# Kernel optimization log

Hardware: AMD Instinct MI355X
Metric: run time of the kernel (lower is better)

## Reference

```python
import jax, jax.numpy as jnp
import numpy as np

N_NODES = 100000
N_EDGES = 1600000
D_IN = 256
H = 4       # n_heads
F = 64      # out_feats per head
NEG_SLOPE = 0.2


def setup_inputs() -> dict:
    key = jax.random.key(0)
    ks = jax.random.split(key, 8)
    feat = jax.random.normal(ks[0], (N_NODES, D_IN), dtype=jnp.float32)
    src = jax.random.randint(ks[1], (N_EDGES,), 0, N_NODES, dtype=jnp.int32)
    dst = jnp.sort(jax.random.randint(ks[2], (N_EDGES,), 0, N_NODES, dtype=jnp.int32))
    s = 1.0 / np.sqrt(D_IN)
    W_src = jax.random.normal(ks[3], (D_IN, H * F), dtype=jnp.float32) * s
    W_dst = jax.random.normal(ks[4], (D_IN, H * F), dtype=jnp.float32) * s
    b_dst = jnp.zeros((H * F,), dtype=jnp.float32)
    Wa_src = jax.random.normal(ks[5], (D_IN, H), dtype=jnp.float32) * s
    Wa_dst = jax.random.normal(ks[6], (D_IN, H), dtype=jnp.float32) * s
    return {"feat": feat, "W_src": W_src, "W_dst": W_dst, "b_dst": b_dst,
            "Wa_src": Wa_src, "Wa_dst": Wa_dst, "src": src, "dst": dst}


def reference(feat, W_src, W_dst, b_dst, Wa_src, Wa_dst, src, dst):
    N = feat.shape[0]
    # node projections
    h_src = (feat @ W_src).reshape(N, H, F)                  # [N,H,F]
    h_dst = (feat @ W_dst + b_dst).reshape(N, H, F)          # residual term
    a_src = feat @ Wa_src                                    # [N,H]
    a_dst = feat @ Wa_dst                                    # [N,H]
    # per-edge attention logits: u_add_v then leaky_relu
    e = a_src[src] + a_dst[dst]                              # [E,H]
    e = jnp.where(e > 0, e, NEG_SLOPE * e)
    # edge softmax grouped by destination node
    emax = jax.ops.segment_max(e, dst, num_segments=N)       # [N,H]
    emax = jnp.where(jnp.isfinite(emax), emax, 0.0)          # empty segments -> 0
    ex = jnp.exp(e - emax[dst])                              # [E,H]
    denom = jax.ops.segment_sum(ex, dst, num_segments=N)     # [N,H]
    a = ex / denom[dst]                                      # [E,H]
    # u_mul_e + sum aggregation
    msg = h_src[src] * a[:, :, None]                         # [E,H,F]
    out = jax.ops.segment_sum(msg, dst, num_segments=N)      # [N,H,F]
    return out + h_dst
```

## Files before the change

### kernel.cpp

```cpp
#include <hip/hip_runtime.h>

#define N_NODES 100000
#define N_EDGES 1600000
#define NEG_SLOPE 0.2f

typedef __bf16 bf16x8 __attribute__((ext_vector_type(8)));
typedef float f32x4 __attribute__((ext_vector_type(4)));
typedef _Float16 f16x4 __attribute__((ext_vector_type(4)));

__device__ inline unsigned short f2bf(float f) {
    union { float f; unsigned u; } x; x.f = f;
    unsigned r = x.u + 0x7fffu + ((x.u >> 16) & 1u);
    return (unsigned short)(r >> 16);
}

__global__ __launch_bounds__(256) void cvt_w_k(const float* __restrict__ Ws,
                                               const float* __restrict__ Wd,
                                               unsigned short* __restrict__ Wsw_src,
                                               unsigned short* __restrict__ Wsw_dst) {
    int idx = blockIdx.x * 256 + threadIdx.x;
    int sel = idx >> 16;
    int r = idx & 65535;
    int k = r >> 8, n = r & 255;
    int ct = n >> 4, nl = n & 15;
    int lane = ((k & 31) >> 3) * 16 + nl, j = k & 7;
    int ks = k >> 5;
    unsigned short v = f2bf((sel == 0 ? Ws : Wd)[k * 256 + n]);
    (sel == 0 ? Wsw_src : Wsw_dst)[(ct * 8 + ks) * 512 + lane * 8 + j] = v;
}

__global__ void cvt_wa_k(const float* __restrict__ Was,
                         const float* __restrict__ Wad,
                         unsigned short* __restrict__ Wa_sw) {
    int idx = blockIdx.x * 256 + threadIdx.x;
    int j = idx & 7, lane = (idx >> 3) & 63, ks = idx >> 9;
    int n = lane & 15, k = ks * 32 + (lane >> 4) * 8 + j;
    float v = n < 4 ? Was[k * 4 + n] : (n < 8 ? Wad[k * 4 + (n - 4)] : 0.f);
    Wa_sw[idx] = f2bf(v);
}

__global__ void rowptr_k(const int* __restrict__ dst, int* __restrict__ rp) {
    int n = blockIdx.x * 256 + threadIdx.x;
    if (n > N_NODES) return;
    int lo = 0, hi = N_EDGES;
    while (lo < hi) { int mid = (lo + hi) >> 1; if (dst[mid] < n) lo = mid + 1; else hi = mid; }
    rp[n] = lo;
}

__global__ __launch_bounds__(256) void aproj_k(const float* __restrict__ feat,
                                               const unsigned short* __restrict__ Wa_sw,
                                               _Float16* __restrict__ a_srcH,
                                               _Float16* __restrict__ a_dstH) {
    int wave = threadIdx.x >> 6, lane = threadIdx.x & 63;
    int quad = lane >> 4, l16 = lane & 15;
    int row_strip = (blockIdx.x * 4 + wave) * 16;
    int arow = row_strip + l16;
    if (arow >= N_NODES) arow = N_NODES - 1;
    const float* arow_p = feat + (size_t)arow * 256;
    const bf16x8* Wa8 = (const bf16x8*)Wa_sw;
    f32x4 acc = {0.f, 0.f, 0.f, 0.f};
    #pragma unroll
    for (int ks = 0; ks < 8; ++ks) {
        int k0 = ks * 32 + quad * 8;
        float4 f0 = *(const float4*)(arow_p + k0);
        float4 f1 = *(const float4*)(arow_p + k0 + 4);
        union { unsigned short u[8]; bf16x8 v; } cv;
        cv.u[0] = f2bf(f0.x); cv.u[1] = f2bf(f0.y);
        cv.u[2] = f2bf(f0.z); cv.u[3] = f2bf(f0.w);
        cv.u[4] = f2bf(f1.x); cv.u[5] = f2bf(f1.y);
        cv.u[6] = f2bf(f1.z); cv.u[7] = f2bf(f1.w);
        acc = __builtin_amdgcn_mfma_f32_16x16x32_bf16(cv.v, Wa8[ks * 64 + lane], acc, 0, 0, 0);
    }
    #pragma unroll
    for (int r = 0; r < 4; ++r) {
        int n = row_strip + quad * 4 + r;
        if (n < N_NODES) {
            if (l16 < 4)      a_srcH[(size_t)n * 4 + l16] = (_Float16)acc[r];
            else if (l16 < 8) a_dstH[(size_t)n * 4 + (l16 - 4)] = (_Float16)acc[r];
        }
    }
}

__global__ __launch_bounds__(512) void proj_k(const float* __restrict__ feat,
                                              const unsigned short* __restrict__ Wsw_src,
                                              const unsigned short* __restrict__ Wsw_dst,
                                              const float* __restrict__ b_dst,
                                              _Float16* __restrict__ h_src,
                                              float* __restrict__ out) {
    __shared__ unsigned short F[4 * 32 * 17 * 8];
    int tid = threadIdx.x, wave = tid >> 6, lane = tid & 63;
    int quad = lane >> 4, l16 = lane & 15;
    int base = blockIdx.x * 64;

    #pragma unroll
    for (int it = 0; it < 8; ++it) {
        int c = tid + it * 512;
        int m = c >> 6, k0 = (c & 63) * 4;
        int row = base + m; if (row > N_NODES - 1) row = N_NODES - 1;
        float4 f = *(const float4*)(feat + (size_t)row * 256 + k0);
        ushort4 u;
        u.x = f2bf(f.x); u.y = f2bf(f.y); u.z = f2bf(f.z); u.w = f2bf(f.w);
        int strip = m >> 4, ms = m & 15, kq = k0 >> 3, jb = k0 & 7;
        *(ushort4*)&F[((strip * 32 + kq) * 17 + ms) * 8 + jb] = u;
    }
    __syncthreads();

    bool isSrc = wave < 4;
    int cg = (wave & 3) * 4;
    const bf16x8* W8 = (const bf16x8*)(isSrc ? Wsw_src : Wsw_dst);

    f32x4 acc[4][4];
    #pragma unroll
    for (int s = 0; s < 4; ++s)
        #pragma unroll
        for (int c = 0; c < 4; ++c) acc[s][c] = (f32x4){0.f, 0.f, 0.f, 0.f};

    #pragma unroll
    for (int ks = 0; ks < 8; ++ks) {
        bf16x8 B0 = W8[((cg + 0) * 8 + ks) * 64 + lane];
        bf16x8 B1 = W8[((cg + 1) * 8 + ks) * 64 + lane];
        bf16x8 B2 = W8[((cg + 2) * 8 + ks) * 64 + lane];
        bf16x8 B3 = W8[((cg + 3) * 8 + ks) * 64 + lane];
        #pragma unroll
        for (int s = 0; s < 4; ++s) {
            bf16x8 A = *(const bf16x8*)&F[((s * 32 + ks * 4 + quad) * 17 + l16) * 8];
            acc[s][0] = __builtin_amdgcn_mfma_f32_16x16x32_bf16(A, B0, acc[s][0], 0, 0, 0);
            acc[s][1] = __builtin_amdgcn_mfma_f32_16x16x32_bf16(A, B1, acc[s][1], 0, 0, 0);
            acc[s][2] = __builtin_amdgcn_mfma_f32_16x16x32_bf16(A, B2, acc[s][2], 0, 0, 0);
            acc[s][3] = __builtin_amdgcn_mfma_f32_16x16x32_bf16(A, B3, acc[s][3], 0, 0, 0);
        }
    }

    if (isSrc) {
        #pragma unroll
        for (int s = 0; s < 4; ++s)
            #pragma unroll
            for (int c = 0; c < 4; ++c) {
                int col = (cg + c) * 16 + l16;
                #pragma unroll
                for (int r = 0; r < 4; ++r) {
                    int row = base + s * 16 + quad * 4 + r;
                    if (row < N_NODES)
                        h_src[(size_t)row * 256 + col] = (_Float16)acc[s][c][r];
                }
            }
    } else {
        #pragma unroll
        for (int c = 0; c < 4; ++c) {
            int col = (cg + c) * 16 + l16;
            float b = b_dst[col];
            #pragma unroll
            for (int s = 0; s < 4; ++s)
                #pragma unroll
                for (int r = 0; r < 4; ++r) {
                    int row = base + s * 16 + quad * 4 + r;
                    if (row < N_NODES)
                        out[(size_t)row * 256 + col] = acc[s][c][r] + b;
                }
        }
    }
}

__global__ __launch_bounds__(256, 6) void agg2_k(const int* __restrict__ src,
                                                 const int* __restrict__ rp,
                                                 const _Float16* __restrict__ a_srcH,
                                                 const _Float16* __restrict__ a_dstH,
                                                 const _Float16* __restrict__ h_src,
                                                 float* __restrict__ out) {
    __shared__ float WT[4][64][4];
    int tid = threadIdx.x, wave = tid >> 6, lane = tid & 63;
    int node = blockIdx.x * 4 + wave;
    int head = lane >> 4;
    int r0 = rp[node], r1 = rp[node + 1], deg = r1 - r0;

    size_t o = (size_t)node * 256 + lane * 4;
    float4 pv = *(const float4*)(out + o);

    f32x4 g = (f32x4){0.f, 0.f, 0.f, 0.f};
    const _Float16* hl = h_src + lane * 4;

    if (deg > 0 && deg <= 64) {
        f16x4 adv4 = *(const f16x4*)(a_dstH + (size_t)node * 4);
        float ad0 = (float)adv4[0], ad1 = (float)adv4[1];
        float ad2 = (float)adv4[2], ad3 = (float)adv4[3];
        bool act = lane < deg;
        int s = 0;
        f16x4 av4 = (f16x4){0, 0, 0, 0};
        if (act) {
            s = src[r0 + lane];
            av4 = *(const f16x4*)(a_srcH + (size_t)s * 4);
        }
        float e0 = (float)av4[0] + ad0; e0 = e0 > 0.f ? e0 : NEG_SLOPE * e0;
        float e1 = (float)av4[1] + ad1; e1 = e1 > 0.f ? e1 : NEG_SLOPE * e1;
        float e2 = (float)av4[2] + ad2; e2 = e2 > 0.f ? e2 : NEG_SLOPE * e2;
        float e3 = (float)av4[3] + ad3; e3 = e3 > 0.f ? e3 : NEG_SLOPE * e3;
        if (!act) { e0 = e1 = e2 = e3 = -1e30f; }
        float m0 = e0, m1 = e1, m2 = e2, m3 = e3;
        for (int off = 1; off < deg; off <<= 1) {
            m0 = fmaxf(m0, __shfl_xor(m0, off));
            m1 = fmaxf(m1, __shfl_xor(m1, off));
            m2 = fmaxf(m2, __shfl_xor(m2, off));
            m3 = fmaxf(m3, __shfl_xor(m3, off));
        }
        float w0 = act ? __expf(e0 - m0) : 0.f;
        float w1 = act ? __expf(e1 - m1) : 0.f;
        float w2 = act ? __expf(e2 - m2) : 0.f;
        float w3 = act ? __expf(e3 - m3) : 0.f;
        float d0 = w0, d1 = w1, d2 = w2, d3 = w3;
        for (int off = 1; off < deg; off <<= 1) {
            d0 += __shfl_xor(d0, off); d1 += __shfl_xor(d1, off);
            d2 += __shfl_xor(d2, off); d3 += __shfl_xor(d3, off);
        }
        w0 *= 1.f / d0; w1 *= 1.f / d1; w2 *= 1.f / d2; w3 *= 1.f / d3;
        float4 wv; wv.x = w0; wv.y = w1; wv.z = w2; wv.w = w3;
        *(float4*)&WT[wave][lane][0] = wv;
        asm volatile("s_waitcnt lgkmcnt(0)" ::: "memory");

        int j = 0;
        for (; j + 4 <= deg; j += 4) {
            int s0 = __builtin_amdgcn_readlane(s, j);
            int s1 = __builtin_amdgcn_readlane(s, j + 1);
            int s2 = __builtin_amdgcn_readlane(s, j + 2);
            int s3 = __builtin_amdgcn_readlane(s, j + 3);
            f16x4 h0 = *(const f16x4*)(hl + (size_t)s0 * 256);
            f16x4 h1 = *(const f16x4*)(hl + (size_t)s1 * 256);
            f16x4 h2 = *(const f16x4*)(hl + (size_t)s2 * 256);
            f16x4 h3 = *(const f16x4*)(hl + (size_t)s3 * 256);
            float x0 = WT[wave][j][head],     x1 = WT[wave][j + 1][head];
            float x2 = WT[wave][j + 2][head], x3 = WT[wave][j + 3][head];
            g[0] += x0 * (float)h0[0]; g[1] += x0 * (float)h0[1];
            g[2] += x0 * (float)h0[2]; g[3] += x0 * (float)h0[3];
            g[0] += x1 * (float)h1[0]; g[1] += x1 * (float)h1[1];
            g[2] += x1 * (float)h1[2]; g[3] += x1 * (float)h1[3];
            g[0] += x2 * (float)h2[0]; g[1] += x2 * (float)h2[1];
            g[2] += x2 * (float)h2[2]; g[3] += x2 * (float)h2[3];
            g[0] += x3 * (float)h3[0]; g[1] += x3 * (float)h3[1];
            g[2] += x3 * (float)h3[2]; g[3] += x3 * (float)h3[3];
        }
        for (; j < deg; ++j) {
            int sj = __builtin_amdgcn_readlane(s, j);
            float xj = WT[wave][j][head];
            f16x4 h = *(const f16x4*)(hl + (size_t)sj * 256);
            g[0] += xj * (float)h[0]; g[1] += xj * (float)h[1];
            g[2] += xj * (float)h[2]; g[3] += xj * (float)h[3];
        }
    } else if (deg > 64) {
        f16x4 adv4 = *(const f16x4*)(a_dstH + (size_t)node * 4);
        float ad0 = (float)adv4[0], ad1 = (float)adv4[1];
        float ad2 = (float)adv4[2], ad3 = (float)adv4[3];
        float m0 = -1e30f, m1 = -1e30f, m2 = -1e30f, m3 = -1e30f;
        for (int e = r0 + lane; e < r1; e += 64) {
            int se = src[e];
            f16x4 av4 = *(const f16x4*)(a_srcH + (size_t)se * 4);
            float e0 = (float)av4[0] + ad0; e0 = e0 > 0.f ? e0 : NEG_SLOPE * e0;
            float e1 = (float)av4[1] + ad1; e1 = e1 > 0.f ? e1 : NEG_SLOPE * e1;
            float e2 = (float)av4[2] + ad2; e2 = e2 > 0.f ? e2 : NEG_SLOPE * e2;
            float e3 = (float)av4[3] + ad3; e3 = e3 > 0.f ? e3 : NEG_SLOPE * e3;
            m0 = fmaxf(m0, e0); m1 = fmaxf(m1, e1);
            m2 = fmaxf(m2, e2); m3 = fmaxf(m3, e3);
        }
        #pragma unroll
        for (int off = 32; off > 0; off >>= 1) {
            m0 = fmaxf(m0, __shfl_xor(m0, off)); m1 = fmaxf(m1, __shfl_xor(m1, off));
            m2 = fmaxf(m2, __shfl_xor(m2, off)); m3 = fmaxf(m3, __shfl_xor(m3, off));
        }
        float d0 = 0.f, d1 = 0.f, d2 = 0.f, d3 = 0.f;
        for (int e = r0 + lane; e < r1; e += 64) {
            int se = src[e];
            f16x4 av4 = *(const f16x4*)(a_srcH + (size_t)se * 4);
            float e0 = (float)av4[0] + ad0; e0 = e0 > 0.f ? e0 : NEG_SLOPE * e0;
            float e1 = (float)av4[1] + ad1; e1 = e1 > 0.f ? e1 : NEG_SLOPE * e1;
            float e2 = (float)av4[2] + ad2; e2 = e2 > 0.f ? e2 : NEG_SLOPE * e2;
            float e3 = (float)av4[3] + ad3; e3 = e3 > 0.f ? e3 : NEG_SLOPE * e3;
            d0 += __expf(e0 - m0); d1 += __expf(e1 - m1);
            d2 += __expf(e2 - m2); d3 += __expf(e3 - m3);
        }
        #pragma unroll
        for (int off = 32; off > 0; off >>= 1) {
            d0 += __shfl_xor(d0, off); d1 += __shfl_xor(d1, off);
            d2 += __shfl_xor(d2, off); d3 += __shfl_xor(d3, off);
        }
        float i0 = 1.f / d0, i1 = 1.f / d1, i2 = 1.f / d2, i3 = 1.f / d3;
        for (int c0 = r0; c0 < r1; c0 += 64) {
            int cnt = min(64, r1 - c0);
            int s = 0; float w0 = 0.f, w1 = 0.f, w2 = 0.f, w3 = 0.f;
            if (lane < cnt) {
                s = src[c0 + lane];
                f16x4 av4 = *(const f16x4*)(a_srcH + (size_t)s * 4);
                float e0 = (float)av4[0] + ad0; e0 = e0 > 0.f ? e0 : NEG_SLOPE * e0;
                float e1 = (float)av4[1] + ad1; e1 = e1 > 0.f ? e1 : NEG_SLOPE * e1;
                float e2 = (float)av4[2] + ad2; e2 = e2 > 0.f ? e2 : NEG_SLOPE * e2;
                float e3 = (float)av4[3] + ad3; e3 = e3 > 0.f ? e3 : NEG_SLOPE * e3;
                w0 = __expf(e0 - m0) * i0; w1 = __expf(e1 - m1) * i1;
                w2 = __expf(e2 - m2) * i2; w3 = __expf(e3 - m3) * i3;
            }
            float4 wv; wv.x = w0; wv.y = w1; wv.z = w2; wv.w = w3;
            *(float4*)&WT[wave][lane][0] = wv;
            asm volatile("s_waitcnt lgkmcnt(0)" ::: "memory");
            for (int j = 0; j < cnt; ++j) {
                int sj = __builtin_amdgcn_readlane(s, j);
                float xj = WT[wave][j][head];
                f16x4 h = *(const f16x4*)(hl + (size_t)sj * 256);
                g[0] += xj * (float)h[0]; g[1] += xj * (float)h[1];
                g[2] += xj * (float)h[2]; g[3] += xj * (float)h[3];
            }
        }
    }
    float4 res;
    res.x = pv.x + g[0]; res.y = pv.y + g[1];
    res.z = pv.z + g[2]; res.w = pv.w + g[3];
    *(float4*)(out + o) = res;
}

extern "C" void kernel_launch(void* const* d_in, const int* in_sizes, int n_in,
                              void* d_out, int out_size, void* d_ws, size_t ws_size,
                              hipStream_t stream) {
    const float* feat   = (const float*)d_in[0];
    const float* W_src  = (const float*)d_in[1];
    const float* W_dst  = (const float*)d_in[2];
    const float* b_dst  = (const float*)d_in[3];
    const float* Wa_src = (const float*)d_in[4];
    const float* Wa_dst = (const float*)d_in[5];
    const int*   src    = (const int*)d_in[6];
    const int*   dst    = (const int*)d_in[7];
    float* out = (float*)d_out;
    char* ws = (char*)d_ws;

    _Float16* h_srcH        = (_Float16*)(ws);
    unsigned short* Wsw_src = (unsigned short*)(ws + 51200000);
    unsigned short* Wsw_dst = (unsigned short*)(ws + 51331072);
    unsigned short* Wa_sw   = (unsigned short*)(ws + 51462144);
    _Float16* a_srcH        = (_Float16*)(ws + 51470336);
    _Float16* a_dstH        = (_Float16*)(ws + 52270336);
    int*      rp            = (int*)(ws + 53070336);

    hipLaunchKernelGGL(cvt_w_k,  dim3(512),   dim3(256), 0, stream, W_src, W_dst, Wsw_src, Wsw_dst);
    hipLaunchKernelGGL(cvt_wa_k, dim3(16),    dim3(256), 0, stream, Wa_src, Wa_dst, Wa_sw);
    hipLaunchKernelGGL(rowptr_k, dim3(391),   dim3(256), 0, stream, dst, rp);
    hipLaunchKernelGGL(aproj_k,  dim3(1563),  dim3(256), 0, stream, feat, Wa_sw, a_srcH, a_dstH);
    hipLaunchKernelGGL(proj_k,   dim3(1563),  dim3(512), 0, stream, feat, Wsw_src, Wsw_dst,
                       b_dst, h_srcH, out);
    hipLaunchKernelGGL(agg2_k,   dim3(25000), dim3(256), 0, stream, src, rp, a_srcH, a_dstH,
                       h_srcH, out);
}
```

Measured before the change: 419.3 us.

## Merge prep kernels, fuse attention projection into proj, store h_dst as fp16

Three small weight-conversion and rowptr kernels become one prep launch, and the attention-logit projection is folded into the main projection kernel as extra blocks, cutting launches from six to three. When the workspace is big enough, the residual h_dst is written as fp16 to a workspace buffer instead of fp32 into out, halving that intermediate write and the read-back in aggregation. This adds fp16 rounding on the residual term and depends on the workspace size at runtime.

Result: faster. 393.7 us (-6.1%).

```diff
diff --git a/kernel.cpp b/kernel.cpp
--- a/kernel.cpp
+++ b/kernel.cpp
@@ -14,84 +14,88 @@
     return (unsigned short)(r >> 16);
 }
 
-__global__ __launch_bounds__(256) void cvt_w_k(const float* __restrict__ Ws,
-                                               const float* __restrict__ Wd,
-                                               unsigned short* __restrict__ Wsw_src,
-                                               unsigned short* __restrict__ Wsw_dst) {
-    int idx = blockIdx.x * 256 + threadIdx.x;
-    int sel = idx >> 16;
-    int r = idx & 65535;
-    int k = r >> 8, n = r & 255;
-    int ct = n >> 4, nl = n & 15;
-    int lane = ((k & 31) >> 3) * 16 + nl, j = k & 7;
-    int ks = k >> 5;
-    unsigned short v = f2bf((sel == 0 ? Ws : Wd)[k * 256 + n]);
-    (sel == 0 ? Wsw_src : Wsw_dst)[(ct * 8 + ks) * 512 + lane * 8 + j] = v;
-}
-
-__global__ void cvt_wa_k(const float* __restrict__ Was,
-                         const float* __restrict__ Wad,
-                         unsigned short* __restrict__ Wa_sw) {
-    int idx = blockIdx.x * 256 + threadIdx.x;
-    int j = idx & 7, lane = (idx >> 3) & 63, ks = idx >> 9;
-    int n = lane & 15, k = ks * 32 + (lane >> 4) * 8 + j;
-    float v = n < 4 ? Was[k * 4 + n] : (n < 8 ? Wad[k * 4 + (n - 4)] : 0.f);
-    Wa_sw[idx] = f2bf(v);
-}
-
-__global__ void rowptr_k(const int* __restrict__ dst, int* __restrict__ rp) {
-    int n = blockIdx.x * 256 + threadIdx.x;
-    if (n > N_NODES) return;
-    int lo = 0, hi = N_EDGES;
-    while (lo < hi) { int mid = (lo + hi) >> 1; if (dst[mid] < n) lo = mid + 1; else hi = mid; }
-    rp[n] = lo;
-}
-
-__global__ __launch_bounds__(256) void aproj_k(const float* __restrict__ feat,
+__global__ __launch_bounds__(256) void prep_k(const float* __restrict__ Ws,
+                                              const float* __restrict__ Wd,
+                                              const float* __restrict__ Was,
+                                              const float* __restrict__ Wad,
+                                              const int* __restrict__ dst,
+                                              unsigned short* __restrict__ Wsw_src,
+                                              unsigned short* __restrict__ Wsw_dst,
+                                              unsigned short* __restrict__ Wa_sw,
+                                              int* __restrict__ rp) {
+    int b = blockIdx.x;
+    if (b < 512) {
+        int idx = b * 256 + threadIdx.x;
+        int sel = idx >> 16;
+        int r = idx & 65535;
+        int k = r >> 8, n = r & 255;
+        int ct = n >> 4, nl = n & 15;
+        int lane = ((k & 31) >> 3) * 16 + nl, j = k & 7;
+        int ks = k >> 5;
+        unsigned short v = f2bf((sel == 0 ? Ws : Wd)[k * 256 + n]);
+        (sel == 0 ? Wsw_src : Wsw_dst)[(ct * 8 + ks) * 512 + lane * 8 + j] = v;
+    } else if (b < 528) {
+        int idx = (b - 512) * 256 + threadIdx.x;
+        int j = idx & 7, lane = (idx >> 3) & 63, ks = idx >> 9;
+        int n = lane & 15, k = ks * 32 + (lane >> 4) * 8 + j;
+        float v = n < 4 ? Was[k * 4 + n] : (n < 8 ? Wad[k * 4 + (n - 4)] : 0.f);
+        Wa_sw[idx] = f2bf(v);
+    } else {
+        int n = (b - 528) * 256 + threadIdx.x;
+        if (n > N_NODES) return;
+        int lo = 0, hi = N_EDGES;
+        while (lo < hi) { int mid = (lo + hi) >> 1; if (dst[mid] < n) lo = mid + 1; else hi = mid; }
+        rp[n] = lo;
+    }
+}
+
+__global__ __launch_bounds__(512) void proja_k(const float* __restrict__ feat,
+                                               const unsigned short* __restrict__ Wsw_src,
+                                               const unsigned short* __restrict__ Wsw_dst,
                                                const unsigned short* __restrict__ Wa_sw,
+                                               const float* __restrict__ b_dst,
+                                               _Float16* __restrict__ h_src,
+                                               _Float16* __restrict__ h_dstH,
+                                               int useHD,
                                                _Float16* __restrict__ a_srcH,
-                                               _Float16* __restrict__ a_dstH) {
-    int wave = threadIdx.x >> 6, lane = threadIdx.x & 63;
-    int quad = lane >> 4, l16 = lane & 15;
-    int row_strip = (blockIdx.x * 4 + wave) * 16;
-    int arow = row_strip + l16;
-    if (arow >= N_NODES) arow = N_NODES - 1;
-    const float* arow_p = feat + (size_t)arow * 256;
-    const bf16x8* Wa8 = (const bf16x8*)Wa_sw;
-    f32x4 acc = {0.f, 0.f, 0.f, 0.f};
-    #pragma unroll
-    for (int ks = 0; ks < 8; ++ks) {
-        int k0 = ks * 32 + quad * 8;
-        float4 f0 = *(const float4*)(arow_p + k0);
-        float4 f1 = *(const float4*)(arow_p + k0 + 4);
-        union { unsigned short u[8]; bf16x8 v; } cv;
-        cv.u[0] = f2bf(f0.x); cv.u[1] = f2bf(f0.y);
-        cv.u[2] = f2bf(f0.z); cv.u[3] = f2bf(f0.w);
-        cv.u[4] = f2bf(f1.x); cv.u[5] = f2bf(f1.y);
-        cv.u[6] = f2bf(f1.z); cv.u[7] = f2bf(f1.w);
-        acc = __builtin_amdgcn_mfma_f32_16x16x32_bf16(cv.v, Wa8[ks * 64 + lane], acc, 0, 0, 0);
-    }
-    #pragma unroll
-    for (int r = 0; r < 4; ++r) {
-        int n = row_strip + quad * 4 + r;
-        if (n < N_NODES) {
-            if (l16 < 4)      a_srcH[(size_t)n * 4 + l16] = (_Float16)acc[r];
-            else if (l16 < 8) a_dstH[(size_t)n * 4 + (l16 - 4)] = (_Float16)acc[r];
-        }
-    }
-}
-
-__global__ __launch_bounds__(512) void proj_k(const float* __restrict__ feat,
-                                              const unsigned short* __restrict__ Wsw_src,
-                                              const unsigned short* __restrict__ Wsw_dst,
-                                              const float* __restrict__ b_dst,
-                                              _Float16* __restrict__ h_src,
-                                              float* __restrict__ out) {
+                                               _Float16* __restrict__ a_dstH,
+                                               float* __restrict__ out) {
     __shared__ unsigned short F[4 * 32 * 17 * 8];
     int tid = threadIdx.x, wave = tid >> 6, lane = tid & 63;
     int quad = lane >> 4, l16 = lane & 15;
+
+    if (blockIdx.x >= 1563) {
+        int strip = (blockIdx.x - 1563) * 8 + wave;
+        int row_strip = strip * 16;
+        int arow = row_strip + l16;
+        if (arow >= N_NODES) arow = N_NODES - 1;
+        const float* arow_p = feat + (size_t)arow * 256;
+        const bf16x8* Wa8 = (const bf16x8*)Wa_sw;
+        f32x4 acc = {0.f, 0.f, 0.f, 0.f};
+        #pragma unroll
+        for (int ks = 0; ks < 8; ++ks) {
+            int k0 = ks * 32 + quad * 8;
+            float4 f0 = *(const float4*)(arow_p + k0);
+            float4 f1 = *(const float4*)(arow_p + k0 + 4);
+            union { unsigned short u[8]; bf16x8 v; } cv;
+            cv.u[0] = f2bf(f0.x); cv.u[1] = f2bf(f0.y);
+            cv.u[2] = f2bf(f0.z); cv.u[3] = f2bf(f0.w);
+            cv.u[4] = f2bf(f1.x); cv.u[5] = f2bf(f1.y);
+            cv.u[6] = f2bf(f1.z); cv.u[7] = f2bf(f1.w);
+            acc = __builtin_amdgcn_mfma_f32_16x16x32_bf16(cv.v, Wa8[ks * 64 + lane], acc, 0, 0, 0);
+        }
+        #pragma unroll
+        for (int r = 0; r < 4; ++r) {
+            int n = row_strip + quad * 4 + r;
+            if (n < N_NODES) {
+                if (l16 < 4)      a_srcH[(size_t)n * 4 + l16] = (_Float16)acc[r];
+                else if (l16 < 8) a_dstH[(size_t)n * 4 + (l16 - 4)] = (_Float16)acc[r];
+            }
+        }
+        return;
+    }
+
     int base = blockIdx.x * 64;
-
     #pragma unroll
     for (int it = 0; it < 8; ++it) {
         int c = tid + it * 512;
@@ -154,8 +158,10 @@
                 #pragma unroll
                 for (int r = 0; r < 4; ++r) {
                     int row = base + s * 16 + quad * 4 + r;
-                    if (row < N_NODES)
-                        out[(size_t)row * 256 + col] = acc[s][c][r] + b;
+                    if (row < N_NODES) {
+                        if (useHD) h_dstH[(size_t)row * 256 + col] = (_Float16)(acc[s][c][r] + b);
+                        else       out[(size_t)row * 256 + col] = acc[s][c][r] + b;
+                    }
                 }
         }
     }
@@ -166,6 +172,8 @@
                                                  const _Float16* __restrict__ a_srcH,
                                                  const _Float16* __restrict__ a_dstH,
                                                  const _Float16* __restrict__ h_src,
+                                                 const _Float16* __restrict__ h_dstH,
+                                                 int useHD,
                                                  float* __restrict__ out) {
     __shared__ float WT[4][64][4];
     int tid = threadIdx.x, wave = tid >> 6, lane = tid & 63;
@@ -174,7 +182,14 @@
     int r0 = rp[node], r1 = rp[node + 1], deg = r1 - r0;
 
     size_t o = (size_t)node * 256 + lane * 4;
-    float4 pv = *(const float4*)(out + o);
+    float4 pv;
+    if (useHD) {
+        f16x4 hd = *(const f16x4*)(h_dstH + o);
+        pv.x = (float)hd[0]; pv.y = (float)hd[1];
+        pv.z = (float)hd[2]; pv.w = (float)hd[3];
+    } else {
+        pv = *(const float4*)(out + o);
+    }
 
     f32x4 g = (f32x4){0.f, 0.f, 0.f, 0.f};
     const _Float16* hl = h_src + lane * 4;
@@ -326,20 +341,34 @@
     float* out = (float*)d_out;
     char* ws = (char*)d_ws;
 
-    _Float16* h_srcH        = (_Float16*)(ws);
-    unsigned short* Wsw_src = (unsigned short*)(ws + 51200000);
-    unsigned short* Wsw_dst = (unsigned short*)(ws + 51331072);
-    unsigned short* Wa_sw   = (unsigned short*)(ws + 51462144);
-    _Float16* a_srcH        = (_Float16*)(ws + 51470336);
-    _Float16* a_dstH        = (_Float16*)(ws + 52270336);
-    int*      rp            = (int*)(ws + 53070336);
-
-    hipLaunchKernelGGL(cvt_w_k,  dim3(512),   dim3(256), 0, stream, W_src, W_dst, Wsw_src, Wsw_dst);
-    hipLaunchKernelGGL(cvt_wa_k, dim3(16),    dim3(256), 0, stream, Wa_src, Wa_dst, Wa_sw);
-    hipLaunchKernelGGL(rowptr_k, dim3(391),   dim3(256), 0, stream, dst, rp);
-    hipLaunchKernelGGL(aproj_k,  dim3(1563),  dim3(256), 0, stream, feat, Wa_sw, a_srcH, a_dstH);
-    hipLaunchKernelGGL(proj_k,   dim3(1563),  dim3(512), 0, stream, feat, Wsw_src, Wsw_dst,
-                       b_dst, h_srcH, out);
-    hipLaunchKernelGGL(agg2_k,   dim3(25000), dim3(256), 0, stream, src, rp, a_srcH, a_dstH,
-                       h_srcH, out);
-}
+    int useHD = ws_size >= 104670340ull ? 1 : 0;
+    _Float16* h_srcH; _Float16* h_dstH;
+    unsigned short *Wsw_src, *Wsw_dst, *Wa_sw;
+    _Float16 *a_srcH, *a_dstH; int* rp;
+    if (useHD) {
+        h_srcH  = (_Float16*)(ws);
+        h_dstH  = (_Float16*)(ws + 51200000);
+        Wsw_src = (unsigned short*)(ws + 102400000);
+        Wsw_dst = (unsigned short*)(ws + 102531072);
+        Wa_sw   = (unsigned short*)(ws + 102662144);
+        a_srcH  = (_Float16*)(ws + 102670336);
+        a_dstH  = (_Float16*)(ws + 103470336);
+        rp      = (int*)(ws + 104270336);
+    } else {
+        h_srcH  = (_Float16*)(ws);
+        h_dstH  = h_srcH;
+        Wsw_src = (unsigned short*)(ws + 51200000);
+        Wsw_dst = (unsigned short*)(ws + 51331072);
+        Wa_sw   = (unsigned short*)(ws + 51462144);
+        a_srcH  = (_Float16*)(ws + 51470336);
+        a_dstH  = (_Float16*)(ws + 52270336);
+        rp      = (int*)(ws + 53070336);
+    }
+
+    hipLaunchKernelGGL(prep_k,  dim3(919),   dim3(256), 0, stream, W_src, W_dst, Wa_src, Wa_dst,
+                       dst, Wsw_src, Wsw_dst, Wa_sw, rp);
+    hipLaunchKernelGGL(proja_k, dim3(2345),  dim3(512), 0, stream, feat, Wsw_src, Wsw_dst,
+                       Wa_sw, b_dst, h_srcH, h_dstH, useHD, a_srcH, a_dstH, out);
+    hipLaunchKernelGGL(agg2_k,  dim3(25000), dim3(256), 0, stream, src, rp, a_srcH, a_dstH,
+                       h_srcH, h_dstH, useHD, out);
+}
```

## Fuse prep kernels and compute attention projections inside main projection kernel

Applied to the files above, without the earlier changes.

Merges the three small setup kernels (weight swizzle, attention-weight swizzle, row-pointer binary search) into one launch that picks its role by block index. Folds the separate attention-logit projection into the main projection kernel, reusing the bf16 feature tile already staged in shared memory, so feat is not read a second time. This cuts three launches and one full pass over the 100 MB feature matrix. In exchange, the source-side waves do extra MFMA work and stores, which lengthens the tail of the projection kernel.

Result: faster. 399.3 us (-4.8%).

```diff
diff --git a/kernel.cpp b/kernel.cpp
--- a/kernel.cpp
+++ b/kernel.cpp
@@ -14,79 +14,50 @@
     return (unsigned short)(r >> 16);
 }
 
-__global__ __launch_bounds__(256) void cvt_w_k(const float* __restrict__ Ws,
-                                               const float* __restrict__ Wd,
-                                               unsigned short* __restrict__ Wsw_src,
-                                               unsigned short* __restrict__ Wsw_dst) {
-    int idx = blockIdx.x * 256 + threadIdx.x;
-    int sel = idx >> 16;
-    int r = idx & 65535;
-    int k = r >> 8, n = r & 255;
-    int ct = n >> 4, nl = n & 15;
-    int lane = ((k & 31) >> 3) * 16 + nl, j = k & 7;
-    int ks = k >> 5;
-    unsigned short v = f2bf((sel == 0 ? Ws : Wd)[k * 256 + n]);
-    (sel == 0 ? Wsw_src : Wsw_dst)[(ct * 8 + ks) * 512 + lane * 8 + j] = v;
-}
-
-__global__ void cvt_wa_k(const float* __restrict__ Was,
-                         const float* __restrict__ Wad,
-                         unsigned short* __restrict__ Wa_sw) {
-    int idx = blockIdx.x * 256 + threadIdx.x;
-    int j = idx & 7, lane = (idx >> 3) & 63, ks = idx >> 9;
-    int n = lane & 15, k = ks * 32 + (lane >> 4) * 8 + j;
-    float v = n < 4 ? Was[k * 4 + n] : (n < 8 ? Wad[k * 4 + (n - 4)] : 0.f);
-    Wa_sw[idx] = f2bf(v);
-}
-
-__global__ void rowptr_k(const int* __restrict__ dst, int* __restrict__ rp) {
-    int n = blockIdx.x * 256 + threadIdx.x;
-    if (n > N_NODES) return;
-    int lo = 0, hi = N_EDGES;
-    while (lo < hi) { int mid = (lo + hi) >> 1; if (dst[mid] < n) lo = mid + 1; else hi = mid; }
-    rp[n] = lo;
-}
-
-__global__ __launch_bounds__(256) void aproj_k(const float* __restrict__ feat,
+__global__ __launch_bounds__(256) void prep_k(const float* __restrict__ Ws,
+                                              const float* __restrict__ Wd,
+                                              const float* __restrict__ Was,
+                                              const float* __restrict__ Wad,
+                                              const int* __restrict__ dst,
+                                              unsigned short* __restrict__ Wsw_src,
+                                              unsigned short* __restrict__ Wsw_dst,
+                                              unsigned short* __restrict__ Wa_sw,
+                                              int* __restrict__ rp) {
+    int b = blockIdx.x;
+    if (b < 512) {
+        int idx = b * 256 + threadIdx.x;
+        int sel = idx >> 16;
+        int r = idx & 65535;
+        int k = r >> 8, n = r & 255;
+        int ct = n >> 4, nl = n & 15;
+        int lane = ((k & 31) >> 3) * 16 + nl, j = k & 7;
+        int ks = k >> 5;
+        unsigned short v = f2bf((sel == 0 ? Ws : Wd)[k * 256 + n]);
+        (sel == 0 ? Wsw_src : Wsw_dst)[(ct * 8 + ks) * 512 + lane * 8 + j] = v;
+    } else if (b < 528) {
+        int idx = (b - 512) * 256 + threadIdx.x;
+        int j = idx & 7, lane = (idx >> 3) & 63, ks = idx >> 9;
+        int n = lane & 15, k = ks * 32 + (lane >> 4) * 8 + j;
+        float v = n < 4 ? Was[k * 4 + n] : (n < 8 ? Wad[k * 4 + (n - 4)] : 0.f);
+        Wa_sw[idx] = f2bf(v);
+    } else {
+        int n = (b - 528) * 256 + threadIdx.x;
+        if (n > N_NODES) return;
+        int lo = 0, hi = N_EDGES;
+        while (lo < hi) { int mid = (lo + hi) >> 1; if (dst[mid] < n) lo = mid + 1; else hi = mid; }
+        rp[n] = lo;
+    }
+}
+
+__global__ __launch_bounds__(512) void proja_k(const float* __restrict__ feat,
+                                               const unsigned short* __restrict__ Wsw_src,
+                                               const unsigned short* __restrict__ Wsw_dst,
                                                const unsigned short* __restrict__ Wa_sw,
+                                               const float* __restrict__ b_dst,
+                                               _Float16* __restrict__ h_src,
                                                _Float16* __restrict__ a_srcH,
-                                               _Float16* __restrict__ a_dstH) {
-    int wave = threadIdx.x >> 6, lane = threadIdx.x & 63;
-    int quad = lane >> 4, l16 = lane & 15;
-    int row_strip = (blockIdx.x * 4 + wave) * 16;
-    int arow = row_strip + l16;
-    if (arow >= N_NODES) arow = N_NODES - 1;
-    const float* arow_p = feat + (size_t)arow * 256;
-    const bf16x8* Wa8 = (const bf16x8*)Wa_sw;
-    f32x4 acc = {0.f, 0.f, 0.f, 0.f};
-    #pragma unroll
-    for (int ks = 0; ks < 8; ++ks) {
-        int k0 = ks * 32 + quad * 8;
-        float4 f0 = *(const float4*)(arow_p + k0);
-        float4 f1 = *(const float4*)(arow_p + k0 + 4);
-        union { unsigned short u[8]; bf16x8 v; } cv;
-        cv.u[0] = f2bf(f0.x); cv.u[1] = f2bf(f0.y);
-        cv.u[2] = f2bf(f0.z); cv.u[3] = f2bf(f0.w);
-        cv.u[4] = f2bf(f1.x); cv.u[5] = f2bf(f1.y);
-        cv.u[6] = f2bf(f1.z); cv.u[7] = f2bf(f1.w);
-        acc = __builtin_amdgcn_mfma_f32_16x16x32_bf16(cv.v, Wa8[ks * 64 + lane], acc, 0, 0, 0);
-    }
-    #pragma unroll
-    for (int r = 0; r < 4; ++r) {
-        int n = row_strip + quad * 4 + r;
-        if (n < N_NODES) {
-            if (l16 < 4)      a_srcH[(size_t)n * 4 + l16] = (_Float16)acc[r];
-            else if (l16 < 8) a_dstH[(size_t)n * 4 + (l16 - 4)] = (_Float16)acc[r];
-        }
-    }
-}
-
-__global__ __launch_bounds__(512) void proj_k(const float* __restrict__ feat,
-                                              const unsigned short* __restrict__ Wsw_src,
-                                              const unsigned short* __restrict__ Wsw_dst,
-                                              const float* __restrict__ b_dst,
-                                              _Float16* __restrict__ h_src,
-                                              float* __restrict__ out) {
+                                               _Float16* __restrict__ a_dstH,
+                                               float* __restrict__ out) {
     __shared__ unsigned short F[4 * 32 * 17 * 8];
     int tid = threadIdx.x, wave = tid >> 6, lane = tid & 63;
     int quad = lane >> 4, l16 = lane & 15;
@@ -132,16 +103,32 @@
     }
 
     if (isSrc) {
-        #pragma unroll
-        for (int s = 0; s < 4; ++s)
+        int s = wave & 3;
+        const bf16x8* Wa8 = (const bf16x8*)Wa_sw;
+        f32x4 acca = (f32x4){0.f, 0.f, 0.f, 0.f};
+        #pragma unroll
+        for (int ks = 0; ks < 8; ++ks) {
+            bf16x8 A = *(const bf16x8*)&F[((s * 32 + ks * 4 + quad) * 17 + l16) * 8];
+            acca = __builtin_amdgcn_mfma_f32_16x16x32_bf16(A, Wa8[ks * 64 + lane], acca, 0, 0, 0);
+        }
+        #pragma unroll
+        for (int r = 0; r < 4; ++r) {
+            int row = base + s * 16 + quad * 4 + r;
+            if (row < N_NODES) {
+                if (l16 < 4)      a_srcH[(size_t)row * 4 + l16] = (_Float16)acca[r];
+                else if (l16 < 8) a_dstH[(size_t)row * 4 + (l16 - 4)] = (_Float16)acca[r];
+            }
+        }
+        #pragma unroll
+        for (int sp = 0; sp < 4; ++sp)
             #pragma unroll
             for (int c = 0; c < 4; ++c) {
                 int col = (cg + c) * 16 + l16;
                 #pragma unroll
                 for (int r = 0; r < 4; ++r) {
-                    int row = base + s * 16 + quad * 4 + r;
+                    int row = base + sp * 16 + quad * 4 + r;
                     if (row < N_NODES)
-                        h_src[(size_t)row * 256 + col] = (_Float16)acc[s][c][r];
+                        h_src[(size_t)row * 256 + col] = (_Float16)acc[sp][c][r];
                 }
             }
     } else {
@@ -150,12 +137,12 @@
             int col = (cg + c) * 16 + l16;
             float b = b_dst[col];
             #pragma unroll
-            for (int s = 0; s < 4; ++s)
+            for (int sp = 0; sp < 4; ++sp)
                 #pragma unroll
                 for (int r = 0; r < 4; ++r) {
-                    int row = base + s * 16 + quad * 4 + r;
+                    int row = base + sp * 16 + quad * 4 + r;
                     if (row < N_NODES)
-                        out[(size_t)row * 256 + col] = acc[s][c][r] + b;
+                        out[(size_t)row * 256 + col] = acc[sp][c][r] + b;
                 }
         }
     }
@@ -334,12 +321,10 @@
     _Float16* a_dstH        = (_Float16*)(ws + 52270336);
     int*      rp            = (int*)(ws + 53070336);
 
-    hipLaunchKernelGGL(cvt_w_k,  dim3(512),   dim3(256), 0, stream, W_src, W_dst, Wsw_src, Wsw_dst);
-    hipLaunchKernelGGL(cvt_wa_k, dim3(16),    dim3(256), 0, stream, Wa_src, Wa_dst, Wa_sw);
-    hipLaunchKernelGGL(rowptr_k, dim3(391),   dim3(256), 0, stream, dst, rp);
-    hipLaunchKernelGGL(aproj_k,  dim3(1563),  dim3(256), 0, stream, feat, Wa_sw, a_srcH, a_dstH);
-    hipLaunchKernelGGL(proj_k,   dim3(1563),  dim3(512), 0, stream, feat, Wsw_src, Wsw_dst,
-                       b_dst, h_srcH, out);
-    hipLaunchKernelGGL(agg2_k,   dim3(25000), dim3(256), 0, stream, src, rp, a_srcH, a_dstH,
+    hipLaunchKernelGGL(prep_k,  dim3(919),   dim3(256), 0, stream, W_src, W_dst, Wa_src, Wa_dst,
+                       dst, Wsw_src, Wsw_dst, Wa_sw, rp);
+    hipLaunchKernelGGL(proja_k, dim3(1563),  dim3(512), 0, stream, feat, Wsw_src, Wsw_dst,
+                       Wa_sw, b_dst, h_srcH, a_srcH, a_dstH, out);
+    hipLaunchKernelGGL(agg2_k,  dim3(25000), dim3(256), 0, stream, src, rp, a_srcH, a_dstH,
                        h_srcH, out);
 }
```
